# Optimization experiments

Measured on AMD Instinct MI355X. Metric: run time of the kernel, lower is better.

Reference implementation:

```python
import jax, jax.numpy as jnp
import numpy as np
import math

S, D, H, L, V = 1024, 768, 12, 6, 32000
KD = D // H
FF = 4 * D
PAD = 0


def setup_inputs() -> dict:
    key = jax.random.key(0)
    ks = jax.random.split(key, 20)
    s = D ** -0.5
    return {
        "token_ids": jax.random.randint(ks[0], (2, S), 0, V, dtype=jnp.int32),
        "emb": jax.random.normal(ks[1], (V, D)) * s,
        "Wq": jax.random.normal(ks[2], (L, H, D, KD)) * s,
        "bq": jnp.zeros((L, H, KD)),
        "Wk": jax.random.normal(ks[3], (L, H, D, KD)) * s,
        "bk": jnp.zeros((L, H, KD)),
        "Wv": jax.random.normal(ks[4], (L, H, D, D)) * s,
        "bv": jnp.zeros((L, H, D)),
        "g1": jnp.ones((L, D)), "be1": jnp.zeros((L, D)),
        "g2": jnp.ones((L, D)), "be2": jnp.zeros((L, D)),
        "W1": jax.random.normal(ks[5], (L, D, FF)) * s,
        "b1": jnp.zeros((L, FF)),
        "W2": jax.random.normal(ks[6], (L, FF, D)) * (FF ** -0.5),
        "b2": jnp.zeros((L, D)),
        "Wout": jax.random.normal(ks[7], (D, V)) * s,
        "bout": jnp.zeros((V,)),
    }


def _pe():
    pos = jnp.arange(S, dtype=jnp.float32)[:, None]
    div = jnp.exp(jnp.arange(0, D, 2, dtype=jnp.float32) * (-math.log(10000.0) / D))
    ang = pos * div  # [S, D/2]
    return jnp.stack([jnp.sin(ang), jnp.cos(ang)], axis=-1).reshape(S, D)


def _ln(x, g, b):
    m = x.mean(-1, keepdims=True)
    v = ((x - m) ** 2).mean(-1, keepdims=True)
    return (x - m) * jax.lax.rsqrt(v + 1e-5) * g + b


def reference(token_ids, emb, Wq, bq, Wk, bk, Wv, bv, g1, be1, g2, be2, W1, b1, W2, b2, Wout, bout):
    pad = token_ids == PAD  # [B,S]
    causal = jnp.triu(jnp.ones((S, S), dtype=bool), k=1)
    # mask[b,s,t] = causal | pad-as-key | pad-as-query
    mask = causal[None, None] | pad[:, None, None, :] | pad[:, None, :, None]  # [B,1,S,S]
    scale = math.sqrt(KD)
    x = emb[token_ids] + _pe()[None]  # [B,S,D]
    for l in range(L):
        q = jnp.einsum('bsd,hdk->bhsk', x, Wq[l]) + bq[l][None, :, None, :]
        k = jnp.einsum('bsd,hdk->bhsk', x, Wk[l]) + bk[l][None, :, None, :]
        v = jnp.einsum('bsd,hde->bhse', x, Wv[l]) + bv[l][None, :, None, :]
        scores = jnp.einsum('bhsk,bhtk->bhst', q, k) / scale
        scores = jnp.where(mask, -jnp.inf, scores)
        all_masked = jnp.all(mask, axis=-1)  # rows with every key masked -> uniform attn
        scores = jnp.where(all_masked[..., None], 0.0, scores)
        attn = jax.nn.softmax(scores, axis=-1)
        heads = jnp.einsum('bhst,bhte->bhse', attn, v)  # per-head full-D values
        attn_out = heads.mean(axis=1)  # heads are AVERAGED, not concatenated
        x = _ln(x + attn_out, g1[l], be1[l])
        ff = jax.nn.relu(x @ W1[l] + b1[l]) @ W2[l] + b2[l]
        x = _ln(x + ff, g2[l], be2[l])
    return x @ Wout + bout
```

## Files before the change

### kernel.cpp

```cpp
#include <hip/hip_runtime.h>
#include <hip/hip_bf16.h>

#define SQ 1024
#define DM 768
#define NH 12
#define NL 6
#define NV 32000
#define KDH 64
#define FFD 3072

using bf16 = __hip_bfloat16;
typedef __attribute__((ext_vector_type(4))) float f32x4;
typedef __attribute__((ext_vector_type(8))) short bf16x8;

__global__ void fill_kernel(float* __restrict__ out, long n, float val) {
  const long stride = (long)gridDim.x * blockDim.x;
  for (long i = (long)blockIdx.x * blockDim.x + threadIdx.x; i < n; i += stride)
    out[i] = val;
}

__device__ __forceinline__ void gload16(const void* g, void* l) {
  __builtin_amdgcn_global_load_lds(
      (const __attribute__((address_space(1))) unsigned int*)g,
      (__attribute__((address_space(3))) unsigned int*)l, 16, 0, 0);
}

template<bool OUT_BF16, bool RELU, bool CSKIP = false, bool CTRUNC = false>
__global__ __launch_bounds__(256) void gemm_bt(
    int M, int N, int K,
    const bf16* __restrict__ Ap, long sAz, int lda,
    const bf16* __restrict__ Bp, long sBz, int ldbt,
    const float* __restrict__ biasp, int sBiasZ,
    void* __restrict__ Cp, long sCz, long sCb, long sCs, long sCn)
{
  __shared__ __align__(16) char lds[49152];

  const int tid = threadIdx.x;
  const int gx = gridDim.x, gy = gridDim.y;
  const int nwg = gx * gy * (int)gridDim.z;
  int flat = ((int)blockIdx.z * gy + (int)blockIdx.y) * gx + (int)blockIdx.x;
  {
    const int q = nwg >> 3, r = nwg & 7;
    const int xcd = flat & 7, loc = flat >> 3;
    flat = (xcd < r ? xcd * (q + 1) : r * (q + 1) + (xcd - r) * q) + loc;
  }
  const int bx  = flat % gx;
  const int byz = flat / gx;
  const int m0 = bx * 128;
  const int n0 = (byz % gy) * 128;
  const int z  = byz / gy;

  if (CSKIP && n0 > m0) return;
  const int KK = CTRUNC ? min(K, m0 + 128) : K;

  const int lane = tid & 63;
  const int wid  = tid >> 6;
  const int wm = (wid >> 1) * 64;
  const int wn = (wid & 1) * 64;

  const int srow  = tid >> 2;
  const int sslot = tid & 3;
  const int xorb  = (sslot ^ (srow & 3)) << 4;

  const char* gA0 = (const char*)(Ap + (long)z * sAz + (long)(m0 + srow) * lda) + xorb;
  const char* gA1 = (const char*)(Ap + (long)z * sAz + (long)(m0 + srow + 64) * lda) + xorb;
  const char* gB0 = (const char*)(Bp + (long)z * sBz + (long)(n0 + srow) * ldbt) + xorb;
  const char* gB1 = (const char*)(Bp + (long)z * sBz + (long)(n0 + srow + 64) * ldbt) + xorb;

  auto stage = [&](int bo) {
    gload16(gA0, lds + bo + tid * 16);
    gload16(gA1, lds + bo + (tid + 256) * 16);
    gload16(gB0, lds + bo + 8192 + tid * 16);
    gload16(gB1, lds + bo + 8192 + (tid + 256) * 16);
    gA0 += 64; gA1 += 64; gB0 += 64; gB1 += 64;
  };

  const int fr = lane & 15;
  const int kq = lane >> 4;
  int fA[4], fB[4];
#pragma unroll
  for (int m = 0; m < 4; ++m) {
    const int R = wm + m * 16 + fr;
    fA[m] = R * 64 + ((kq ^ (R & 3)) << 4);
  }
#pragma unroll
  for (int n = 0; n < 4; ++n) {
    const int R = wn + n * 16 + fr;
    fB[n] = 8192 + R * 64 + ((kq ^ (R & 3)) << 4);
  }

  f32x4 acc[4][4] = {};

  const int nt = KK >> 5;
  stage(0);
  stage(16384);
  int cur = 0;
  for (int t = 0; t < nt; ++t) {
    if (t + 2 < nt) {
      int nb = cur + 2; if (nb >= 3) nb -= 3;
      stage(nb * 16384);
      asm volatile("s_waitcnt vmcnt(8)" ::: "memory");
    } else if (t + 1 < nt) {
      asm volatile("s_waitcnt vmcnt(4)" ::: "memory");
    } else {
      asm volatile("s_waitcnt vmcnt(0)" ::: "memory");
    }
    __builtin_amdgcn_s_barrier();
    const int co = cur * 16384;
    bf16x8 af[4], bfr[4];
#pragma unroll
    for (int m = 0; m < 4; ++m) af[m] = *(const bf16x8*)(lds + co + fA[m]);
#pragma unroll
    for (int n = 0; n < 4; ++n) bfr[n] = *(const bf16x8*)(lds + co + fB[n]);
#pragma unroll
    for (int m = 0; m < 4; ++m)
#pragma unroll
      for (int n = 0; n < 4; ++n)
        acc[m][n] = __builtin_amdgcn_mfma_f32_16x16x32_bf16(af[m], bfr[n], acc[m][n], 0, 0, 0);
    __builtin_amdgcn_s_barrier();
    cur = (cur == 2) ? 0 : cur + 1;
  }

  const int rg = (lane >> 4) * 4;
  const int cl = lane & 15;
  const long zb = (long)z * sBiasZ;
#pragma unroll
  for (int n = 0; n < 4; ++n) {
    const int gcol = n0 + wn + n * 16 + cl;
    const float bias = biasp ? biasp[zb + gcol] : 0.f;
    if (OUT_BF16 && sCs == 1) {
#pragma unroll
      for (int m = 0; m < 4; ++m) {
        const int grow = m0 + wm + m * 16 + rg;
        const long ci = (long)z * sCz + (long)(grow >> 10) * sCb
                      + (long)(grow & 1023) + (long)gcol * sCn;
        ushort4 pk;
        float v0 = acc[m][n][0] + bias, v1 = acc[m][n][1] + bias;
        float v2 = acc[m][n][2] + bias, v3 = acc[m][n][3] + bias;
        if (RELU) { v0 = fmaxf(v0, 0.f); v1 = fmaxf(v1, 0.f);
                    v2 = fmaxf(v2, 0.f); v3 = fmaxf(v3, 0.f); }
        pk.x = __builtin_bit_cast(ushort, __float2bfloat16(v0));
        pk.y = __builtin_bit_cast(ushort, __float2bfloat16(v1));
        pk.z = __builtin_bit_cast(ushort, __float2bfloat16(v2));
        pk.w = __builtin_bit_cast(ushort, __float2bfloat16(v3));
        *(ushort4*)((bf16*)Cp + ci) = pk;
      }
    } else {
#pragma unroll
      for (int m = 0; m < 4; ++m) {
#pragma unroll
        for (int rr = 0; rr < 4; ++rr) {
          const int grow = m0 + wm + m * 16 + rg + rr;
          float v = acc[m][n][rr] + bias;
          if (RELU) v = fmaxf(v, 0.f);
          const long ci = (long)z * sCz + (long)(grow >> 10) * sCb
                        + (long)(grow & 1023) * sCs + (long)gcol * sCn;
          if (OUT_BF16) ((bf16*)Cp)[ci] = __float2bfloat16(v);
          else          ((float*)Cp)[ci] = v;
        }
      }
    }
  }
}

__global__ __launch_bounds__(256) void transpose_kernel(
    const float* __restrict__ in, long sInZ, int ldin,
    bf16* __restrict__ out, long sOutZ, int ldout)
{
  __shared__ float t[64][65];
  const int tid = threadIdx.x;
  const int n0 = blockIdx.x * 64, k0 = blockIdx.y * 64;
  const float* ip = in + (long)blockIdx.z * sInZ;
  bf16* op = out + (long)blockIdx.z * sOutZ;
  const int cx = (tid & 15) * 4, ry = tid >> 4;
#pragma unroll
  for (int p = 0; p < 4; ++p) {
    const int k = ry + p * 16;
    const float4 v = *(const float4*)(ip + (long)(k0 + k) * ldin + n0 + cx);
    t[k][cx] = v.x; t[k][cx + 1] = v.y; t[k][cx + 2] = v.z; t[k][cx + 3] = v.w;
  }
  __syncthreads();
#pragma unroll
  for (int p = 0; p < 4; ++p) {
    const int n = ry + p * 16;
    ushort4 o;
    o.x = __builtin_bit_cast(ushort, __float2bfloat16(t[cx + 0][n]));
    o.y = __builtin_bit_cast(ushort, __float2bfloat16(t[cx + 1][n]));
    o.z = __builtin_bit_cast(ushort, __float2bfloat16(t[cx + 2][n]));
    o.w = __builtin_bit_cast(ushort, __float2bfloat16(t[cx + 3][n]));
    *(ushort4*)(op + (long)(n0 + n) * ldout + k0 + cx) = o;
  }
}

__global__ void biasqk_kernel(const float* __restrict__ bq, const float* __restrict__ bk,
                              float* __restrict__ out) {
  const int i = blockIdx.x * 256 + threadIdx.x;
  if (i < NH * 128) {
    const int h = i >> 7, n = i & 127;
    out[i] = (n < 64) ? bq[h * 64 + n] : bk[h * 64 + n - 64];
  }
}

__global__ __launch_bounds__(256) void xpart_kernel(
    const float* __restrict__ x, float* __restrict__ xpart) {
  const int b = blockIdx.x, g = blockIdx.y;
  const int tid = threadIdx.x;
  const float* xp = x + (long)b * SQ * DM + (long)g * 64 * DM;
  float a0 = 0.f, a1 = 0.f, a2 = 0.f;
  for (int s = 0; s < 64; ++s) {
    a0 += xp[(long)s * DM + tid];
    a1 += xp[(long)s * DM + tid + 256];
    a2 += xp[(long)s * DM + tid + 512];
  }
  float* op = xpart + (long)(b * 16 + g) * DM;
  op[tid] = a0; op[tid + 256] = a1; op[tid + 512] = a2;
}

__global__ void xmeanf_kernel(const float* __restrict__ xpart, float* __restrict__ xmean) {
  const int b = blockIdx.x;
  const int d = threadIdx.x;
  float a = 0.f;
#pragma unroll
  for (int g = 0; g < 16; ++g) a += xpart[(long)(b * 16 + g) * DM + d];
  xmean[b * DM + d] = a * (1.0f / (float)SQ);
}

__global__ __launch_bounds__(256) void vmeanw_kernel(
    const float* __restrict__ xmean, const bf16* __restrict__ wvT,
    const float* __restrict__ bv, float* __restrict__ vmean) {
  const int tid = threadIdx.x;
  const int w = blockIdx.x * 4 + (tid >> 6);
  const int b = w / DM;
  const int e = w % DM;
  const int lane = tid & 63;
  float xm[12];
#pragma unroll
  for (int j = 0; j < 12; ++j) xm[j] = xmean[b * DM + lane + j * 64];
  float acc = 0.f;
  for (int h = 0; h < NH; ++h) {
    const bf16* wr = wvT + ((long)h * DM + e) * DM;
#pragma unroll
    for (int j = 0; j < 12; ++j)
      acc += xm[j] * __bfloat162float(wr[lane + j * 64]);
  }
#pragma unroll
  for (int o = 32; o >= 1; o >>= 1) acc += __shfl_xor(acc, o);
  if (lane == 0) {
    float bs = 0.f;
#pragma unroll
    for (int h = 0; h < NH; ++h) bs += bv[h * DM + e];
    vmean[b * DM + e] = (acc + bs) * (1.0f / (float)NH);
  }
}

__global__ __launch_bounds__(256) void embed_kernel(
    const int* __restrict__ tok, const float* __restrict__ emb,
    float* __restrict__ x, bf16* __restrict__ xb)
{
  const int gid = blockIdx.x * 256 + threadIdx.x;
  const int row = gid / (DM / 4);
  const int dc  = (gid % (DM / 4)) * 4;
  const int t = tok[row];
  const int s = row & (SQ - 1);
#pragma unroll
  for (int j = 0; j < 4; ++j) {
    const int d = dc + j;
    const float e = emb[(long)t * DM + d];
    const float div = expf(-(float)(d & ~1) * (9.210340371976184f / (float)DM));
    const float ang = (float)s * div;
    const float pe = (d & 1) ? cosf(ang) : sinf(ang);
    const float v = e + pe;
    x[(long)row * DM + d] = v;
    xb[(long)row * DM + d] = __float2bfloat16(v);
  }
}

__global__ __launch_bounds__(256) void softmax_kernel(
    bf16* __restrict__ P, const int* __restrict__ tok)
{
  const int row = blockIdx.x;
  const int s = row & (SQ - 1);
  const int z = row >> 10;
  const int b = z / NH;
  const int* tb = tok + b * SQ;
  if (tb[s] == 0) return;
  bf16* sp = P + (long)row * SQ;
  const int tid = threadIdx.x;
  const int t0 = tid * 4;
  const int L = (s | 127) + 1;
  const bool act = t0 < L;

  float val[4] = {-1e30f, -1e30f, -1e30f, -1e30f};
  float vmax = -1e30f;
  if (act) {
    uint2 raw = *(const uint2*)(sp + t0);
    int4 tv = *(const int4*)(tb + t0);
    const bf16* rh = (const bf16*)&raw;
    const int tvv[4] = {tv.x, tv.y, tv.z, tv.w};
#pragma unroll
    for (int j = 0; j < 4; ++j) {
      const int t = t0 + j;
      const bool valid = (t <= s) && (tvv[j] != 0);
      val[j] = valid ? __bfloat162float(rh[j]) * 0.125f : -1e30f;
      vmax = fmaxf(vmax, val[j]);
    }
  }
  __shared__ float red[4];
  const int lane = tid & 63, wid = tid >> 6;
  float w = vmax;
#pragma unroll
  for (int o = 32; o >= 1; o >>= 1) w = fmaxf(w, __shfl_xor(w, o));
  if (lane == 0) red[wid] = w;
  __syncthreads();
  const float Mx = fmaxf(fmaxf(red[0], red[1]), fmaxf(red[2], red[3]));
  __syncthreads();
  float e[4]; float lsum = 0.f;
#pragma unroll
  for (int j = 0; j < 4; ++j) {
    e[j] = (val[j] > -1e29f) ? expf(val[j] - Mx) : 0.f;
    lsum += e[j];
  }
  w = lsum;
#pragma unroll
  for (int o = 32; o >= 1; o >>= 1) w += __shfl_xor(w, o);
  if (lane == 0) red[wid] = w;
  __syncthreads();
  const float inv = 1.0f / (red[0] + red[1] + red[2] + red[3]);
  if (act) {
    ushort4 pk;
    pk.x = __builtin_bit_cast(ushort, __float2bfloat16(e[0] * inv));
    pk.y = __builtin_bit_cast(ushort, __float2bfloat16(e[1] * inv));
    pk.z = __builtin_bit_cast(ushort, __float2bfloat16(e[2] * inv));
    pk.w = __builtin_bit_cast(ushort, __float2bfloat16(e[3] * inv));
    *(ushort4*)(sp + t0) = pk;
  }
}

template<int MODE>
__global__ __launch_bounds__(256) void ln_kernel(
    float* __restrict__ x, bf16* __restrict__ xb,
    const float* __restrict__ tmp, const bf16* __restrict__ heads,
    const float* __restrict__ g, const float* __restrict__ be,
    const int* __restrict__ tok, const float* __restrict__ vmean)
{
  const int r = blockIdx.x;
  const int b = r >> 10;
  const int s = r & (SQ - 1);
  const int tid = threadIdx.x;
  __shared__ float rs[4], rq[4];
  const bool pad = (MODE == 1) && (tok[r] == 0);
  float sum = 0.f, sq = 0.f;
  float v[8];
  if (tid < 96) {
    const int d0 = tid * 8;
    const float4 x0 = *(const float4*)(x + (long)r * DM + d0);
    const float4 x1 = *(const float4*)(x + (long)r * DM + d0 + 4);
    v[0] = x0.x; v[1] = x0.y; v[2] = x0.z; v[3] = x0.w;
    v[4] = x1.x; v[5] = x1.y; v[6] = x1.z; v[7] = x1.w;
    if (MODE == 0) {
      const float4 t0_ = *(const float4*)(tmp + (long)r * DM + d0);
      const float4 t1_ = *(const float4*)(tmp + (long)r * DM + d0 + 4);
      v[0] += t0_.x; v[1] += t0_.y; v[2] += t0_.z; v[3] += t0_.w;
      v[4] += t1_.x; v[5] += t1_.y; v[6] += t1_.z; v[7] += t1_.w;
    } else if (pad) {
      const float4 t0_ = *(const float4*)(vmean + b * DM + d0);
      const float4 t1_ = *(const float4*)(vmean + b * DM + d0 + 4);
      v[0] += t0_.x; v[1] += t0_.y; v[2] += t0_.z; v[3] += t0_.w;
      v[4] += t1_.x; v[5] += t1_.y; v[6] += t1_.z; v[7] += t1_.w;
    } else {
      float hs[8] = {0.f, 0.f, 0.f, 0.f, 0.f, 0.f, 0.f, 0.f};
      for (int h = 0; h < NH; ++h) {
        union { uint4 u; ushort us[8]; } hv;
        hv.u = *(const uint4*)(heads + ((long)(b * NH + h) * SQ + s) * DM + d0);
#pragma unroll
        for (int j = 0; j < 8; ++j)
          hs[j] += __bfloat162float(__builtin_bit_cast(bf16, hv.us[j]));
      }
#pragma unroll
      for (int j = 0; j < 8; ++j) v[j] += hs[j] * (1.0f / (float)NH);
    }
#pragma unroll
    for (int j = 0; j < 8; ++j) { sum += v[j]; sq += v[j] * v[j]; }
  }
  const int lane = tid & 63, wid = tid >> 6;
  float s1 = sum, s2 = sq;
#pragma unroll
  for (int o = 32; o >= 1; o >>= 1) { s1 += __shfl_xor(s1, o); s2 += __shfl_xor(s2, o); }
  if (lane == 0) { rs[wid] = s1; rq[wid] = s2; }
  __syncthreads();
  const float S1 = rs[0] + rs[1] + rs[2] + rs[3];
  const float S2 = rq[0] + rq[1] + rq[2] + rq[3];
  const float mean = S1 * (1.0f / (float)DM);
  const float var  = S2 * (1.0f / (float)DM) - mean * mean;
  const float rstd = rsqrtf(var + 1e-5f);
  if (tid < 96) {
    const int d0 = tid * 8;
    const float4 g0 = *(const float4*)(g + d0);
    const float4 g1 = *(const float4*)(g + d0 + 4);
    const float4 b0 = *(const float4*)(be + d0);
    const float4 b1 = *(const float4*)(be + d0 + 4);
    float o[8];
    o[0] = (v[0] - mean) * rstd * g0.x + b0.x;
    o[1] = (v[1] - mean) * rstd * g0.y + b0.y;
    o[2] = (v[2] - mean) * rstd * g0.z + b0.z;
    o[3] = (v[3] - mean) * rstd * g0.w + b0.w;
    o[4] = (v[4] - mean) * rstd * g1.x + b1.x;
    o[5] = (v[5] - mean) * rstd * g1.y + b1.y;
    o[6] = (v[6] - mean) * rstd * g1.z + b1.z;
    o[7] = (v[7] - mean) * rstd * g1.w + b1.w;
    *(float4*)(x + (long)r * DM + d0)     = make_float4(o[0], o[1], o[2], o[3]);
    *(float4*)(x + (long)r * DM + d0 + 4) = make_float4(o[4], o[5], o[6], o[7]);
    union { uint4 u; ushort us[8]; } pk;
#pragma unroll
    for (int j = 0; j < 8; ++j)
      pk.us[j] = __builtin_bit_cast(ushort, __float2bfloat16(o[j]));
    *(uint4*)(xb + (long)r * DM + d0) = pk.u;
  }
}

extern "C" void kernel_launch(void* const* d_in, const int* in_sizes, int n_in,
                              void* d_out, int out_size, void* d_ws, size_t ws_size,
                              hipStream_t stream) {
  const int expect_sizes[18] = {
    2048, 24576000, 3538944, 4608, 3538944, 4608, 42467328, 55296,
    4608, 4608, 4608, 4608, 14155776, 18432, 14155776, 4608, 24576000, 32000
  };
  bool sizes_ok = (n_in == 18);
  if (sizes_ok)
    for (int i = 0; i < 18; ++i) sizes_ok = sizes_ok && (in_sizes[i] == expect_sizes[i]);
  if (!sizes_ok) {
    fill_kernel<<<2048, 256, 0, stream>>>((float*)d_out, (long)out_size, 1000.0f);
    return;
  }
  if (out_size != 65536000) {
    fill_kernel<<<2048, 256, 0, stream>>>((float*)d_out, (long)out_size, 3000.0f);
    return;
  }
  if (ws_size < 158189568ull) {
    fill_kernel<<<2048, 256, 0, stream>>>((float*)d_out, (long)out_size, 2000.0f);
    return;
  }

  const int*   tok  = (const int*)d_in[0];
  const float* emb  = (const float*)d_in[1];
  const float* Wq   = (const float*)d_in[2];
  const float* bq   = (const float*)d_in[3];
  const float* Wk   = (const float*)d_in[4];
  const float* bk   = (const float*)d_in[5];
  const float* Wv   = (const float*)d_in[6];
  const float* bv   = (const float*)d_in[7];
  const float* g1   = (const float*)d_in[8];
  const float* be1  = (const float*)d_in[9];
  const float* g2   = (const float*)d_in[10];
  const float* be2  = (const float*)d_in[11];
  const float* W1   = (const float*)d_in[12];
  const float* b1   = (const float*)d_in[13];
  const float* W2   = (const float*)d_in[14];
  const float* b2   = (const float*)d_in[15];
  const float* Wout = (const float*)d_in[16];
  const float* bout = (const float*)d_in[17];

  char* ws = (char*)d_ws;
  float* x      = (float*)(ws + 0);
  bf16*  xb     = (bf16*) (ws + 6291456);
  bf16*  qk     = (bf16*) (ws + 9437184);
  float* tmp    = (float*)(ws + 9437184);
  bf16*  vT     = (bf16*) (ws + 15728640);
  bf16*  P      = (bf16*) (ws + 53477376);
  bf16*  ff     = (bf16*) (ws + 53477376);
  bf16*  woutT  = (bf16*) (ws + 53477376);
  bf16*  heads  = (bf16*) (ws + 103809024);
  bf16*  wqkT   = (bf16*) (ws + 141557760);
  bf16*  wvT    = (bf16*) (ws + 143917056);
  bf16*  w1T    = (bf16*) (ws + 141557760);
  bf16*  w2T    = (bf16*) (ws + 146276352);
  float* biasqk = (float*)(ws + 158072832);
  float* xpart  = (float*)(ws + 158078976);
  float* xmean  = (float*)(ws + 158177280);
  float* vmean  = (float*)(ws + 158183424);

  embed_kernel<<<dim3((2 * SQ * DM / 4) / 256), 256, 0, stream>>>(tok, emb, x, xb);

  for (int l = 0; l < NL; ++l) {
    transpose_kernel<<<dim3(1, 12, NH), 256, 0, stream>>>(
        Wq + (long)l * NH * DM * KDH, (long)DM * KDH, KDH,
        wqkT, 128 * DM, DM);
    transpose_kernel<<<dim3(1, 12, NH), 256, 0, stream>>>(
        Wk + (long)l * NH * DM * KDH, (long)DM * KDH, KDH,
        wqkT + 64 * DM, 128 * DM, DM);
    transpose_kernel<<<dim3(12, 12, NH), 256, 0, stream>>>(
        Wv + (long)l * NH * DM * DM, (long)DM * DM, DM,
        wvT, (long)DM * DM, DM);
    biasqk_kernel<<<6, 256, 0, stream>>>(bq + l * NH * KDH, bk + l * NH * KDH, biasqk);

    xpart_kernel<<<dim3(2, 16), 256, 0, stream>>>(x, xpart);
    xmeanf_kernel<<<dim3(2), 768, 0, stream>>>(xpart, xmean);
    vmeanw_kernel<<<dim3(384), 256, 0, stream>>>(xmean, wvT, bv + (long)l * NH * DM, vmean);

    gemm_bt<true, false><<<dim3(16, 1, NH), 256, 0, stream>>>(
        2048, 128, DM, xb, 0, DM, wqkT, (long)128 * DM, DM,
        biasqk, 128,
        qk, (long)SQ * 128, (long)NH * SQ * 128, 128, 1);
    gemm_bt<true, false><<<dim3(16, 6, NH), 256, 0, stream>>>(
        2048, DM, DM, xb, 0, DM, wvT, (long)DM * DM, DM,
        bv + (long)l * NH * DM, DM,
        vT, (long)DM * SQ, (long)NH * DM * SQ, 1, SQ);
    gemm_bt<true, false, true, false><<<dim3(8, 8, 2 * NH), 256, 0, stream>>>(
        SQ, SQ, KDH, qk, (long)SQ * 128, 128, qk + 64, (long)SQ * 128, 128,
        (const float*)nullptr, 0,
        P, (long)SQ * SQ, 0, SQ, 1);
    softmax_kernel<<<dim3(2 * NH * SQ), 256, 0, stream>>>(P, tok);
    gemm_bt<true, false, false, true><<<dim3(8, 6, 2 * NH), 256, 0, stream>>>(
        SQ, DM, SQ, P, (long)SQ * SQ, SQ, vT, (long)DM * SQ, SQ,
        (const float*)nullptr, 0,
        heads, (long)SQ * DM, 0, DM, 1);
    ln_kernel<1><<<dim3(2048), 256, 0, stream>>>(x, xb, nullptr, heads,
                                                 g1 + l * DM, be1 + l * DM, tok, vmean);
    transpose_kernel<<<dim3(48, 12, 1), 256, 0, stream>>>(
        W1 + (long)l * DM * FFD, 0, FFD, w1T, 0, DM);
    transpose_kernel<<<dim3(12, 48, 1), 256, 0, stream>>>(
        W2 + (long)l * FFD * DM, 0, DM, w2T, 0, FFD);
    gemm_bt<true, true><<<dim3(16, 24, 1), 256, 0, stream>>>(
        2048, FFD, DM, xb, 0, DM, w1T, 0, DM,
        b1 + (long)l * FFD, 0,
        ff, 0, (long)SQ * FFD, FFD, 1);
    gemm_bt<false, false><<<dim3(16, 6, 1), 256, 0, stream>>>(
        2048, DM, FFD, ff, 0, FFD, w2T, 0, FFD,
        b2 + (long)l * DM, 0,
        tmp, 0, (long)SQ * DM, DM, 1);
    ln_kernel<0><<<dim3(2048), 256, 0, stream>>>(x, xb, tmp, nullptr,
                                                 g2 + l * DM, be2 + l * DM, tok, nullptr);
  }
  transpose_kernel<<<dim3(500, 12, 1), 256, 0, stream>>>(Wout, 0, NV, woutT, 0, DM);
  gemm_bt<false, false><<<dim3(16, 250, 1), 256, 0, stream>>>(
      2048, NV, DM, xb, 0, DM, woutT, 0, DM,
      bout, 0,
      d_out, 0, (long)SQ * NV, NV, 1);
}
```

Before: 1.708 ms.

## Split-K FF2 GEMM, triangular QK grid, and fuse prep kernels

The FF2 GEMM is split four ways along K, each slice writing its own fp32 partial buffer, and the LayerNorm kernel sums the partials and adds the bias. This gives 384 workgroups instead of 96. The QK^T GEMM now launches only the lower-triangular tiles, using sqrt-based index decoding, instead of launching the full grid and returning early. The weight-transpose and bias kernels are merged into one prep kernel per stage, and the x-mean reduction is folded into vmeanw, cutting launch count at the cost of redundant reads and extra partial-buffer traffic.

```diff
diff --git a/kernel.cpp b/kernel.cpp
--- a/kernel.cpp
+++ b/kernel.cpp
@@ -25,7 +25,7 @@
       (__attribute__((address_space(3))) unsigned int*)l, 16, 0, 0);
 }
 
-template<bool OUT_BF16, bool RELU, bool CSKIP = false, bool CTRUNC = false>
+template<bool OUT_BF16, bool RELU, bool TRI = false, bool CTRUNC = false>
 __global__ __launch_bounds__(256) void gemm_bt(
     int M, int N, int K,
     const bf16* __restrict__ Ap, long sAz, int lda,
@@ -44,13 +44,22 @@
     const int xcd = flat & 7, loc = flat >> 3;
     flat = (xcd < r ? xcd * (q + 1) : r * (q + 1) + (xcd - r) * q) + loc;
   }
-  const int bx  = flat % gx;
-  const int byz = flat / gx;
-  const int m0 = bx * 128;
-  const int n0 = (byz % gy) * 128;
-  const int z  = byz / gy;
-
-  if (CSKIP && n0 > m0) return;
+  int m0, n0, z;
+  if (TRI) {
+    z = flat / 36;
+    const int t = flat % 36;
+    int i = (int)((sqrtf(8.0f * (float)t + 1.0f) - 1.0f) * 0.5f);
+    if ((i + 1) * (i + 2) / 2 <= t) ++i;
+    if (i * (i + 1) / 2 > t) --i;
+    const int j = t - i * (i + 1) / 2;
+    m0 = i * 128; n0 = j * 128;
+  } else {
+    const int bx  = flat % gx;
+    const int byz = flat / gx;
+    m0 = bx * 128;
+    n0 = (byz % gy) * 128;
+    z  = byz / gy;
+  }
   const int KK = CTRUNC ? min(K, m0 + 128) : K;
 
   const int lane = tid & 63;
@@ -163,20 +172,16 @@
   }
 }
 
-__global__ __launch_bounds__(256) void transpose_kernel(
-    const float* __restrict__ in, long sInZ, int ldin,
-    bf16* __restrict__ out, long sOutZ, int ldout)
+__device__ __forceinline__ void transpose_tile(
+    const float* __restrict__ in, int ldin, bf16* __restrict__ out, int ldout,
+    int n0, int k0, int tid)
 {
   __shared__ float t[64][65];
-  const int tid = threadIdx.x;
-  const int n0 = blockIdx.x * 64, k0 = blockIdx.y * 64;
-  const float* ip = in + (long)blockIdx.z * sInZ;
-  bf16* op = out + (long)blockIdx.z * sOutZ;
   const int cx = (tid & 15) * 4, ry = tid >> 4;
 #pragma unroll
   for (int p = 0; p < 4; ++p) {
     const int k = ry + p * 16;
-    const float4 v = *(const float4*)(ip + (long)(k0 + k) * ldin + n0 + cx);
+    const float4 v = *(const float4*)(in + (long)(k0 + k) * ldin + n0 + cx);
     t[k][cx] = v.x; t[k][cx + 1] = v.y; t[k][cx + 2] = v.z; t[k][cx + 3] = v.w;
   }
   __syncthreads();
@@ -188,16 +193,61 @@
     o.y = __builtin_bit_cast(ushort, __float2bfloat16(t[cx + 1][n]));
     o.z = __builtin_bit_cast(ushort, __float2bfloat16(t[cx + 2][n]));
     o.w = __builtin_bit_cast(ushort, __float2bfloat16(t[cx + 3][n]));
-    *(ushort4*)(op + (long)(n0 + n) * ldout + k0 + cx) = o;
-  }
-}
-
-__global__ void biasqk_kernel(const float* __restrict__ bq, const float* __restrict__ bk,
-                              float* __restrict__ out) {
-  const int i = blockIdx.x * 256 + threadIdx.x;
-  if (i < NH * 128) {
-    const int h = i >> 7, n = i & 127;
-    out[i] = (n < 64) ? bq[h * 64 + n] : bk[h * 64 + n - 64];
+    *(ushort4*)(out + (long)(n0 + n) * ldout + k0 + cx) = o;
+  }
+}
+
+__global__ __launch_bounds__(256) void transpose_kernel(
+    const float* __restrict__ in, long sInZ, int ldin,
+    bf16* __restrict__ out, long sOutZ, int ldout)
+{
+  transpose_tile(in + (long)blockIdx.z * sInZ, ldin,
+                 out + (long)blockIdx.z * sOutZ, ldout,
+                 blockIdx.x * 64, blockIdx.y * 64, threadIdx.x);
+}
+
+__global__ __launch_bounds__(256) void prep_attn_kernel(
+    const float* __restrict__ Wq_l, const float* __restrict__ Wk_l,
+    const float* __restrict__ Wv_l,
+    const float* __restrict__ bq_l, const float* __restrict__ bk_l,
+    bf16* __restrict__ wqkT, bf16* __restrict__ wvT, float* __restrict__ biasqk)
+{
+  const int tid = threadIdx.x;
+  int f = blockIdx.x;
+  if (f < 144) {
+    const int h = f / 12, ky = f % 12;
+    transpose_tile(Wq_l + (long)h * DM * KDH, KDH,
+                   wqkT + (long)h * 128 * DM, DM, 0, ky * 64, tid);
+  } else if (f < 288) {
+    f -= 144;
+    const int h = f / 12, ky = f % 12;
+    transpose_tile(Wk_l + (long)h * DM * KDH, KDH,
+                   wqkT + (long)h * 128 * DM + (long)64 * DM, DM, 0, ky * 64, tid);
+  } else if (f < 2016) {
+    f -= 288;
+    const int h = f / 144, r = f % 144;
+    transpose_tile(Wv_l + (long)h * DM * DM, DM,
+                   wvT + (long)h * DM * DM, DM, (r % 12) * 64, (r / 12) * 64, tid);
+  } else {
+    const int i = (f - 2016) * 256 + tid;
+    if (i < NH * 128) {
+      const int h = i >> 7, n = i & 127;
+      biasqk[i] = (n < 64) ? bq_l[h * 64 + n] : bk_l[h * 64 + n - 64];
+    }
+  }
+}
+
+__global__ __launch_bounds__(256) void prep_ff_kernel(
+    const float* __restrict__ W1_l, const float* __restrict__ W2_l,
+    bf16* __restrict__ w1T, bf16* __restrict__ w2T)
+{
+  const int tid = threadIdx.x;
+  int f = blockIdx.x;
+  if (f < 576) {
+    transpose_tile(W1_l, FFD, w1T, DM, (f % 48) * 64, (f / 48) * 64, tid);
+  } else {
+    f -= 576;
+    transpose_tile(W2_l, DM, w2T, FFD, (f % 12) * 64, (f / 12) * 64, tid);
   }
 }
 
@@ -216,17 +266,8 @@
   op[tid] = a0; op[tid + 256] = a1; op[tid + 512] = a2;
 }
 
-__global__ void xmeanf_kernel(const float* __restrict__ xpart, float* __restrict__ xmean) {
-  const int b = blockIdx.x;
-  const int d = threadIdx.x;
-  float a = 0.f;
-#pragma unroll
-  for (int g = 0; g < 16; ++g) a += xpart[(long)(b * 16 + g) * DM + d];
-  xmean[b * DM + d] = a * (1.0f / (float)SQ);
-}
-
 __global__ __launch_bounds__(256) void vmeanw_kernel(
-    const float* __restrict__ xmean, const bf16* __restrict__ wvT,
+    const float* __restrict__ xpart, const bf16* __restrict__ wvT,
     const float* __restrict__ bv, float* __restrict__ vmean) {
   const int tid = threadIdx.x;
   const int w = blockIdx.x * 4 + (tid >> 6);
@@ -235,7 +276,13 @@
   const int lane = tid & 63;
   float xm[12];
 #pragma unroll
-  for (int j = 0; j < 12; ++j) xm[j] = xmean[b * DM + lane + j * 64];
+  for (int j = 0; j < 12; ++j) {
+    float a = 0.f;
+#pragma unroll
+    for (int g = 0; g < 16; ++g)
+      a += xpart[(long)(b * 16 + g) * DM + lane + j * 64];
+    xm[j] = a * (1.0f / (float)SQ);
+  }
   float acc = 0.f;
   for (int h = 0; h < NH; ++h) {
     const bf16* wr = wvT + ((long)h * DM + e) * DM;
@@ -336,12 +383,14 @@
   }
 }
 
+#define TCHUNK 1572864L
 template<int MODE>
 __global__ __launch_bounds__(256) void ln_kernel(
     float* __restrict__ x, bf16* __restrict__ xb,
     const float* __restrict__ tmp, const bf16* __restrict__ heads,
     const float* __restrict__ g, const float* __restrict__ be,
-    const int* __restrict__ tok, const float* __restrict__ vmean)
+    const int* __restrict__ tok, const float* __restrict__ vmean,
+    const float* __restrict__ bias)
 {
   const int r = blockIdx.x;
   const int b = r >> 10;
@@ -358,10 +407,18 @@
     v[0] = x0.x; v[1] = x0.y; v[2] = x0.z; v[3] = x0.w;
     v[4] = x1.x; v[5] = x1.y; v[6] = x1.z; v[7] = x1.w;
     if (MODE == 0) {
-      const float4 t0_ = *(const float4*)(tmp + (long)r * DM + d0);
-      const float4 t1_ = *(const float4*)(tmp + (long)r * DM + d0 + 4);
-      v[0] += t0_.x; v[1] += t0_.y; v[2] += t0_.z; v[3] += t0_.w;
-      v[4] += t1_.x; v[5] += t1_.y; v[6] += t1_.z; v[7] += t1_.w;
+#pragma unroll
+      for (int c = 0; c < 4; ++c) {
+        const float* tp = tmp + c * TCHUNK + (long)r * DM + d0;
+        const float4 t0_ = *(const float4*)tp;
+        const float4 t1_ = *(const float4*)(tp + 4);
+        v[0] += t0_.x; v[1] += t0_.y; v[2] += t0_.z; v[3] += t0_.w;
+        v[4] += t1_.x; v[5] += t1_.y; v[6] += t1_.z; v[7] += t1_.w;
+      }
+      const float4 b0_ = *(const float4*)(bias + d0);
+      const float4 b1_ = *(const float4*)(bias + d0 + 4);
+      v[0] += b0_.x; v[1] += b0_.y; v[2] += b0_.z; v[3] += b0_.w;
+      v[4] += b1_.x; v[5] += b1_.y; v[6] += b1_.z; v[7] += b1_.w;
     } else if (pad) {
       const float4 t0_ = *(const float4*)(vmean + b * DM + d0);
       const float4 t1_ = *(const float4*)(vmean + b * DM + d0 + 4);
@@ -464,10 +521,9 @@
   float* x      = (float*)(ws + 0);
   bf16*  xb     = (bf16*) (ws + 6291456);
   bf16*  qk     = (bf16*) (ws + 9437184);
-  float* tmp    = (float*)(ws + 9437184);
   bf16*  vT     = (bf16*) (ws + 15728640);
+  float* tmp    = (float*)(ws + 15728640);
   bf16*  P      = (bf16*) (ws + 53477376);
-  bf16*  ff     = (bf16*) (ws + 53477376);
   bf16*  woutT  = (bf16*) (ws + 53477376);
   bf16*  heads  = (bf16*) (ws + 103809024);
   bf16*  wqkT   = (bf16*) (ws + 141557760);
@@ -476,26 +532,19 @@
   bf16*  w2T    = (bf16*) (ws + 146276352);
   float* biasqk = (float*)(ws + 158072832);
   float* xpart  = (float*)(ws + 158078976);
-  float* xmean  = (float*)(ws + 158177280);
   float* vmean  = (float*)(ws + 158183424);
 
   embed_kernel<<<dim3((2 * SQ * DM / 4) / 256), 256, 0, stream>>>(tok, emb, x, xb);
 
   for (int l = 0; l < NL; ++l) {
-    transpose_kernel<<<dim3(1, 12, NH), 256, 0, stream>>>(
-        Wq + (long)l * NH * DM * KDH, (long)DM * KDH, KDH,
-        wqkT, 128 * DM, DM);
-    transpose_kernel<<<dim3(1, 12, NH), 256, 0, stream>>>(
-        Wk + (long)l * NH * DM * KDH, (long)DM * KDH, KDH,
-        wqkT + 64 * DM, 128 * DM, DM);
-    transpose_kernel<<<dim3(12, 12, NH), 256, 0, stream>>>(
-        Wv + (long)l * NH * DM * DM, (long)DM * DM, DM,
-        wvT, (long)DM * DM, DM);
-    biasqk_kernel<<<6, 256, 0, stream>>>(bq + l * NH * KDH, bk + l * NH * KDH, biasqk);
+    prep_attn_kernel<<<dim3(2022), 256, 0, stream>>>(
+        Wq + (long)l * NH * DM * KDH, Wk + (long)l * NH * DM * KDH,
+        Wv + (long)l * NH * DM * DM,
+        bq + l * NH * KDH, bk + l * NH * KDH,
+        wqkT, wvT, biasqk);
 
     xpart_kernel<<<dim3(2, 16), 256, 0, stream>>>(x, xpart);
-    xmeanf_kernel<<<dim3(2), 768, 0, stream>>>(xpart, xmean);
-    vmeanw_kernel<<<dim3(384), 256, 0, stream>>>(xmean, wvT, bv + (long)l * NH * DM, vmean);
+    vmeanw_kernel<<<dim3(384), 256, 0, stream>>>(xpart, wvT, bv + (long)l * NH * DM, vmean);
 
     gemm_bt<true, false><<<dim3(16, 1, NH), 256, 0, stream>>>(
         2048, 128, DM, xb, 0, DM, wqkT, (long)128 * DM, DM,
@@ -505,7 +554,7 @@
         2048, DM, DM, xb, 0, DM, wvT, (long)DM * DM, DM,
         bv + (long)l * NH * DM, DM,
         vT, (long)DM * SQ, (long)NH * DM * SQ, 1, SQ);
-    gemm_bt<true, false, true, false><<<dim3(8, 8, 2 * NH), 256, 0, stream>>>(
+    gemm_bt<true, false, true, false><<<dim3(36, 1, 2 * NH), 256, 0, stream>>>(
         SQ, SQ, KDH, qk, (long)SQ * 128, 128, qk + 64, (long)SQ * 128, 128,
         (const float*)nullptr, 0,
         P, (long)SQ * SQ, 0, SQ, 1);
@@ -515,21 +564,21 @@
         (const float*)nullptr, 0,
         heads, (long)SQ * DM, 0, DM, 1);
     ln_kernel<1><<<dim3(2048), 256, 0, stream>>>(x, xb, nullptr, heads,
-                                                 g1 + l * DM, be1 + l * DM, tok, vmean);
-    transpose_kernel<<<dim3(48, 12, 1), 256, 0, stream>>>(
-        W1 + (long)l * DM * FFD, 0, FFD, w1T, 0, DM);
-    transpose_kernel<<<dim3(12, 48, 1), 256, 0, stream>>>(
-        W2 + (long)l * FFD * DM, 0, DM, w2T, 0, FFD);
+                                                 g1 + l * DM, be1 + l * DM, tok, vmean,
+                                                 nullptr);
+    prep_ff_kernel<<<dim3(1152), 256, 0, stream>>>(
+        W1 + (long)l * DM * FFD, W2 + (long)l * FFD * DM, w1T, w2T);
     gemm_bt<true, true><<<dim3(16, 24, 1), 256, 0, stream>>>(
         2048, FFD, DM, xb, 0, DM, w1T, 0, DM,
         b1 + (long)l * FFD, 0,
-        ff, 0, (long)SQ * FFD, FFD, 1);
-    gemm_bt<false, false><<<dim3(16, 6, 1), 256, 0, stream>>>(
-        2048, DM, FFD, ff, 0, FFD, w2T, 0, FFD,
-        b2 + (long)l * DM, 0,
-        tmp, 0, (long)SQ * DM, DM, 1);
+        (bf16*)P, 0, (long)SQ * FFD, FFD, 1);
+    gemm_bt<false, false><<<dim3(16, 6, 4), 256, 0, stream>>>(
+        2048, DM, 768, (bf16*)P, 768, FFD, w2T, 768, FFD,
+        (const float*)nullptr, 0,
+        tmp, TCHUNK, (long)SQ * DM, DM, 1);
     ln_kernel<0><<<dim3(2048), 256, 0, stream>>>(x, xb, tmp, nullptr,
-                                                 g2 + l * DM, be2 + l * DM, tok, nullptr);
+                                                 g2 + l * DM, be2 + l * DM, tok, nullptr,
+                                                 b2 + (long)l * DM);
   }
   transpose_kernel<<<dim3(500, 12, 1), 256, 0, stream>>>(Wout, 0, NV, woutT, 0, DM);
   gemm_bt<false, false><<<dim3(16, 250, 1), 256, 0, stream>>>(
```

Result: faster. 1.584 ms (-7.3%).
